# Kernel optimization log

Measured on AMD Instinct MI355X. Metric: run time of the kernel, lower is better.

## Reference

```python
import jax, jax.numpy as jnp
import numpy as np

N_NODES = 100000
N_EDGES = 6400000
D_FEAT = 5
OUT_CLASSES = 16


def setup_inputs() -> dict:
    key = jax.random.key(0)
    k1, k2, k3, k4, k5 = jax.random.split(key, 5)
    h = jax.random.normal(k1, (N_NODES, D_FEAT), dtype=jnp.float32)
    src = jax.random.randint(k2, (N_EDGES,), 0, N_NODES, dtype=jnp.int64)
    dst = jax.random.randint(k3, (N_EDGES,), 0, N_NODES, dtype=jnp.int64)
    W_weight = jax.random.normal(k4, (OUT_CLASSES, 2 * D_FEAT), dtype=jnp.float32) * 0.1
    W_bias = jax.random.normal(k5, (OUT_CLASSES,), dtype=jnp.float32) * 0.1
    return {"h": h, "src": src, "dst": dst, "W_weight": W_weight, "W_bias": W_bias}


def reference(h, src, dst, W_weight, W_bias):
    # Edge-wise: gather src/dst node features, concat -> [E, 2D], linear -> [E, C]
    h_u = h[src]                      # [E, D]
    h_v = h[dst]                      # [E, D]
    feat = jnp.concatenate([h_u, h_v], axis=1)  # [E, 2D]
    score = feat @ W_weight.T + W_bias           # [E, C]
    return score
```

## Files before the change

### kernel.cpp

```cpp
#include <hip/hip_runtime.h>


typedef float f4v __attribute__((ext_vector_type(4)));
typedef f4v uf4v __attribute__((aligned(4)));

constexpr int C = 16;
constexpr int TWO_D = 10;

template <int CTRL>
__device__ __forceinline__ float qperm(float x) {
    return __int_as_float(
        __builtin_amdgcn_mov_dpp(__float_as_int(x), CTRL, 0xF, 0xF, true));
}

__global__ __launch_bounds__(256) void edge_mlp_v3(
    const float* __restrict__ h,
    const int* __restrict__ src,
    const int* __restrict__ dst,
    const float* __restrict__ Ww,
    const float* __restrict__ Wb,
    float* __restrict__ out,
    int totalItems)
{
    __shared__ float sW[C * TWO_D + C];
    for (int i = threadIdx.x; i < C * TWO_D + C; i += blockDim.x)
        sW[i] = (i < C * TWO_D) ? Ww[i] : Wb[i - C * TWO_D];
    __syncthreads();

    const int tid0 = blockIdx.x * blockDim.x + threadIdx.x;
    const int q = tid0 & 3;
    const bool odd = (q & 1) != 0;
    const bool isV = (q >= 2);

    float w[4][TWO_D], bias[4];
#pragma unroll
    for (int j = 0; j < 4; ++j) {
        const int c = q * 4 + j;
#pragma unroll
        for (int k = 0; k < TWO_D; ++k) w[j][k] = sW[c * TWO_D + k];
        bias[j] = sW[C * TWO_D + c];
    }

    const int stride = gridDim.x * blockDim.x;
    const int stride2 = stride * 2;
    const int TImax = totalItems - 1;

    auto clampE = [&](int g) { return (g < TImax ? g : TImax) >> 2; };

    auto loadrow = [&](int s, int d) -> f4v {
        const int r = isV ? d : s;
        const float* p = h + (size_t)r * 5 + (odd ? 1 : 0);
        return *reinterpret_cast<const uf4v*>(p);
    };

    auto body = [&](const f4v m, int gout, bool doStore) {
        const float o0 = qperm<0xB1>(m[0]);
        const float o3 = qperm<0xB1>(m[3]);
        const float a0 = odd ? o0   : m[0];
        const float a1 = odd ? m[0] : m[1];
        const float a2 = odd ? m[1] : m[2];
        const float a3 = odd ? m[2] : m[3];
        const float a4 = odd ? m[3] : o3;
        const float b0 = qperm<0x4E>(a0);
        const float b1 = qperm<0x4E>(a1);
        const float b2 = qperm<0x4E>(a2);
        const float b3 = qperm<0x4E>(a3);
        const float b4 = qperm<0x4E>(a4);

        const float u0 = isV ? b0 : a0, v0 = isV ? a0 : b0;
        const float u1 = isV ? b1 : a1, v1 = isV ? a1 : b1;
        const float u2 = isV ? b2 : a2, v2 = isV ? a2 : b2;
        const float u3 = isV ? b3 : a3, v3 = isV ? a3 : b3;
        const float u4 = isV ? b4 : a4, v4 = isV ? a4 : b4;

        f4v r;
#pragma unroll
        for (int j = 0; j < 4; ++j) {
            float a = bias[j];
            a += u0 * w[j][0] + u1 * w[j][1] + u2 * w[j][2] + u3 * w[j][3] + u4 * w[j][4];
            a += v0 * w[j][5] + v1 * w[j][6] + v2 * w[j][7] + v3 * w[j][8] + v4 * w[j][9];
            r[j] = a;
        }
        if (doStore)
            __builtin_nontemporal_store(r, reinterpret_cast<f4v*>(out + (size_t)gout * 4));
    };

    int eA = clampE(tid0), eB = clampE(tid0 + stride);
    int sA = __builtin_nontemporal_load(src + eA);
    int dA = __builtin_nontemporal_load(dst + eA);
    int sB = __builtin_nontemporal_load(src + eB);
    int dB = __builtin_nontemporal_load(dst + eB);
    f4v gA = loadrow(sA, dA);
    f4v gB = loadrow(sB, dB);
    {
        const int gn = tid0 + stride2;
        eA = clampE(gn); eB = clampE(gn + stride);
        sA = __builtin_nontemporal_load(src + eA);
        dA = __builtin_nontemporal_load(dst + eA);
        sB = __builtin_nontemporal_load(src + eB);
        dB = __builtin_nontemporal_load(dst + eB);
    }

    for (int g = tid0; g < totalItems; g += stride2) {
        const f4v nA = loadrow(sA, dA);
        const f4v nB = loadrow(sB, dB);
        const int gn = g + 2 * stride2;
        eA = clampE(gn); eB = clampE(gn + stride);
        sA = __builtin_nontemporal_load(src + eA);
        dA = __builtin_nontemporal_load(dst + eA);
        sB = __builtin_nontemporal_load(src + eB);
        dB = __builtin_nontemporal_load(dst + eB);
        body(gA, g, true);
        body(gB, g + stride, (g + stride) < totalItems);
        gA = nA; gB = nB;
    }
}

extern "C" void kernel_launch(void* const* d_in, const int* in_sizes, int n_in,
                              void* d_out, int out_size, void* d_ws, size_t ws_size,
                              hipStream_t stream) {
    const float* h   = (const float*)d_in[0];
    const int*   src = (const int*)d_in[1];
    const int*   dst = (const int*)d_in[2];
    const float* Ww  = (const float*)d_in[3];
    const float* Wb  = (const float*)d_in[4];
    float* out = (float*)d_out;

    const int E = in_sizes[1];
    const int totalItems = E * 4;

    edge_mlp_v3<<<4096, 256, 0, stream>>>(h, src, dst, Ww, Wb, out, totalItems);
}
```

Baseline: 555.2 us.

## Precompute per-node projected table, reduce edge kernel to gather-add

Splits the linear layer by linearity: a first kernel computes, for every node, W_u·h+b and W_v·h (32 floats per row) into workspace, and the edge kernel gathers the two 16-float halves and adds them. This removes the per-edge FMAs and DPP shuffles and makes the gathers aligned float4 loads. The cost is a 12.8 MB table whose gathered rows are larger than the original 20-byte feature rows, plus an extra launch. The fallback kernel, used only when the workspace is missing or too small, is simplified to drop its software prefetching.

New measurement: 597.0 us. 1.08x slower.

```diff
diff --git a/kernel.cpp b/kernel.cpp
--- a/kernel.cpp
+++ b/kernel.cpp
@@ -5,7 +5,94 @@
 typedef f4v uf4v __attribute__((aligned(4)));
 
 constexpr int C = 16;
+constexpr int D = 5;
 constexpr int TWO_D = 10;
+constexpr int ROW = 32;
+
+__global__ __launch_bounds__(256) void build_table(
+    const float* __restrict__ h, const float* __restrict__ Ww,
+    const float* __restrict__ Wb, float* __restrict__ P, int nNodes)
+{
+    const int n = blockIdx.x * blockDim.x + threadIdx.x;
+    if (n >= nNodes) return;
+    float hh[D];
+#pragma unroll
+    for (int k = 0; k < D; ++k) hh[k] = h[(size_t)n * D + k];
+
+    float rowbuf[ROW];
+#pragma unroll
+    for (int c = 0; c < C; ++c) {
+        float pu = Wb[c];
+        float pv = 0.0f;
+#pragma unroll
+        for (int k = 0; k < D; ++k) {
+            pu += hh[k] * Ww[c * TWO_D + k];
+            pv += hh[k] * Ww[c * TWO_D + D + k];
+        }
+        rowbuf[c] = pu;
+        rowbuf[C + c] = pv;
+    }
+    f4v* dst = reinterpret_cast<f4v*>(P + (size_t)n * ROW);
+#pragma unroll
+    for (int j = 0; j < ROW / 4; ++j)
+        dst[j] = *reinterpret_cast<const f4v*>(&rowbuf[j * 4]);
+}
+
+__global__ __launch_bounds__(256) void edge_add(
+    const float* __restrict__ P,
+    const int* __restrict__ src,
+    const int* __restrict__ dst,
+    float* __restrict__ out,
+    int totalItems)
+{
+    const int tid0 = blockIdx.x * blockDim.x + threadIdx.x;
+    const int qoff = (tid0 & 3) * 4;
+    const int stride = gridDim.x * blockDim.x;
+    const int stride2 = stride * 2;
+    const int TImax = totalItems - 1;
+
+    auto clampE = [&](int g) { return (g < TImax ? g : TImax) >> 2; };
+    auto gatherU = [&](int s) -> f4v {
+        return *reinterpret_cast<const f4v*>(P + (size_t)s * ROW + qoff);
+    };
+    auto gatherV = [&](int d) -> f4v {
+        return *reinterpret_cast<const f4v*>(P + (size_t)d * ROW + C + qoff);
+    };
+
+    int eA = clampE(tid0), eB = clampE(tid0 + stride);
+    int sA = __builtin_nontemporal_load(src + eA);
+    int dA = __builtin_nontemporal_load(dst + eA);
+    int sB = __builtin_nontemporal_load(src + eB);
+    int dB = __builtin_nontemporal_load(dst + eB);
+    f4v uA = gatherU(sA), vA = gatherV(dA);
+    f4v uB = gatherU(sB), vB = gatherV(dB);
+    {
+        const int gn = tid0 + stride2;
+        eA = clampE(gn); eB = clampE(gn + stride);
+        sA = __builtin_nontemporal_load(src + eA);
+        dA = __builtin_nontemporal_load(dst + eA);
+        sB = __builtin_nontemporal_load(src + eB);
+        dB = __builtin_nontemporal_load(dst + eB);
+    }
+
+    for (int g = tid0; g < totalItems; g += stride2) {
+        const f4v nuA = gatherU(sA), nvA = gatherV(dA);
+        const f4v nuB = gatherU(sB), nvB = gatherV(dB);
+        const int gn = g + 2 * stride2;
+        eA = clampE(gn); eB = clampE(gn + stride);
+        sA = __builtin_nontemporal_load(src + eA);
+        dA = __builtin_nontemporal_load(dst + eA);
+        sB = __builtin_nontemporal_load(src + eB);
+        dB = __builtin_nontemporal_load(dst + eB);
+        const f4v rA = uA + vA;
+        __builtin_nontemporal_store(rA, reinterpret_cast<f4v*>(out + (size_t)g * 4));
+        if (g + stride < totalItems) {
+            const f4v rB = uB + vB;
+            __builtin_nontemporal_store(rB, reinterpret_cast<f4v*>(out + (size_t)(g + stride) * 4));
+        }
+        uA = nuA; vA = nvA; uB = nuB; vB = nvB;
+    }
+}
 
 template <int CTRL>
 __device__ __forceinline__ float qperm(float x) {
@@ -42,18 +129,12 @@
     }
 
     const int stride = gridDim.x * blockDim.x;
-    const int stride2 = stride * 2;
-    const int TImax = totalItems - 1;
+    for (int g = tid0; g < totalItems; g += stride) {
+        const int e = g >> 2;
+        const int r = isV ? dst[e] : src[e];
+        const float* p = h + (size_t)r * D + (odd ? 1 : 0);
+        const f4v m = *reinterpret_cast<const uf4v*>(p);
 
-    auto clampE = [&](int g) { return (g < TImax ? g : TImax) >> 2; };
-
-    auto loadrow = [&](int s, int d) -> f4v {
-        const int r = isV ? d : s;
-        const float* p = h + (size_t)r * 5 + (odd ? 1 : 0);
-        return *reinterpret_cast<const uf4v*>(p);
-    };
-
-    auto body = [&](const f4v m, int gout, bool doStore) {
         const float o0 = qperm<0xB1>(m[0]);
         const float o3 = qperm<0xB1>(m[3]);
         const float a0 = odd ? o0   : m[0];
@@ -73,46 +154,15 @@
         const float u3 = isV ? b3 : a3, v3 = isV ? a3 : b3;
         const float u4 = isV ? b4 : a4, v4 = isV ? a4 : b4;
 
-        f4v r;
+        f4v r4;
 #pragma unroll
         for (int j = 0; j < 4; ++j) {
             float a = bias[j];
             a += u0 * w[j][0] + u1 * w[j][1] + u2 * w[j][2] + u3 * w[j][3] + u4 * w[j][4];
             a += v0 * w[j][5] + v1 * w[j][6] + v2 * w[j][7] + v3 * w[j][8] + v4 * w[j][9];
-            r[j] = a;
+            r4[j] = a;
         }
-        if (doStore)
-            __builtin_nontemporal_store(r, reinterpret_cast<f4v*>(out + (size_t)gout * 4));
-    };
-
-    int eA = clampE(tid0), eB = clampE(tid0 + stride);
-    int sA = __builtin_nontemporal_load(src + eA);
-    int dA = __builtin_nontemporal_load(dst + eA);
-    int sB = __builtin_nontemporal_load(src + eB);
-    int dB = __builtin_nontemporal_load(dst + eB);
-    f4v gA = loadrow(sA, dA);
-    f4v gB = loadrow(sB, dB);
-    {
-        const int gn = tid0 + stride2;
-        eA = clampE(gn); eB = clampE(gn + stride);
-        sA = __builtin_nontemporal_load(src + eA);
-        dA = __builtin_nontemporal_load(dst + eA);
-        sB = __builtin_nontemporal_load(src + eB);
-        dB = __builtin_nontemporal_load(dst + eB);
-    }
-
-    for (int g = tid0; g < totalItems; g += stride2) {
-        const f4v nA = loadrow(sA, dA);
-        const f4v nB = loadrow(sB, dB);
-        const int gn = g + 2 * stride2;
-        eA = clampE(gn); eB = clampE(gn + stride);
-        sA = __builtin_nontemporal_load(src + eA);
-        dA = __builtin_nontemporal_load(dst + eA);
-        sB = __builtin_nontemporal_load(src + eB);
-        dB = __builtin_nontemporal_load(dst + eB);
-        body(gA, g, true);
-        body(gB, g + stride, (g + stride) < totalItems);
-        gA = nA; gB = nB;
+        __builtin_nontemporal_store(r4, reinterpret_cast<f4v*>(out + (size_t)g * 4));
     }
 }
 
@@ -128,6 +178,14 @@
 
     const int E = in_sizes[1];
     const int totalItems = E * 4;
+    const int nNodes = in_sizes[0] / D;
 
-    edge_mlp_v3<<<4096, 256, 0, stream>>>(h, src, dst, Ww, Wb, out, totalItems);
+    const size_t needWs = (size_t)nNodes * ROW * sizeof(float);
+    if (d_ws != nullptr && ws_size >= needWs) {
+        float* P = (float*)d_ws;
+        build_table<<<(nNodes + 255) / 256, 256, 0, stream>>>(h, Ww, Wb, P, nNodes);
+        edge_add<<<4096, 256, 0, stream>>>(P, src, dst, out, totalItems);
+    } else {
+        edge_mlp_v3<<<4096, 256, 0, stream>>>(h, src, dst, Ww, Wb, out, totalItems);
+    }
 }
```
